# Kernel tuning notes

Measured on AMD Instinct MI355X. Metric: run time of the kernel, lower is better.

## Reference

```python
import jax, jax.numpy as jnp
import numpy as np

LAMBDA_VIOLATION = 0.5
NUM_SAMPLES = 128
EPS = 1e-09
B = 4096
K_MAX = 128
NK_MAX = 128
# unique (n, k, m) parameter combos, cycled over the batch
COMBOS = np.array([[256, 128, 3], [192, 96, 3], [224, 112, 4], [160, 80, 2]], dtype=np.int64)


def setup_inputs() -> dict:
    key = jax.random.key(0)
    k1, k2, k3 = jax.random.split(key, 3)
    y_pred = jax.random.uniform(k1, (B, 1), minval=0.5, maxval=8.0, dtype=jnp.float32)
    y_true = jax.random.uniform(k2, (B, 1), minval=0.5, maxval=8.0, dtype=jnp.float32)
    P_padded = jax.random.normal(k3, (B, K_MAX, NK_MAX), dtype=jnp.float32)
    params = jnp.asarray(COMBOS[np.arange(B) % len(COMBOS)])  # [B, 3] int64
    return {"y_pred": y_pred, "y_true": y_true, "P_padded": P_padded, "params": params}


def reference(y_pred, y_true, P_padded, params):
    # LogMSE in base 2
    log2_pred = jnp.log2(jnp.clip(y_pred, EPS))
    log2_true = jnp.log2(jnp.clip(y_true, EPS))
    loss_logmse = jnp.mean((log2_true - log2_pred) ** 2)

    batch = P_padded.shape[0]
    p_np = np.asarray(params)  # int params are concrete constants
    combos, inverse = np.unique(p_np, axis=0, return_inverse=True)

    total_penalty = jnp.asarray(0.0, dtype=y_pred.dtype)
    xkey = jax.random.key(42)
    for i in range(combos.shape[0]):
        n, k, m = int(combos[i, 0]), int(combos[i, 1]), int(combos[i, 2])
        idx = np.nonzero(inverse == i)[0]
        if m + 1 > n or k <= 0 or n - k < 0 or idx.size == 0:
            continue
        g = idx.size
        P_actual = P_padded[idx, :k, : n - k]            # [g, k, n-k]
        X = jax.random.normal(jax.random.fold_in(xkey, i), (g, NUM_SAMPLES, k), dtype=y_pred.dtype)
        # G = [I_k | P_actual]  =>  C = X @ G = [X | X @ P_actual]
        C = jnp.concatenate([X, jnp.einsum('bsk,bkp->bsp', X, P_actual)], axis=2)  # [g, S, n]
        mags = jnp.abs(C)
        top, _ = jax.lax.top_k(mags, m + 1)              # [g, S, m+1] sorted descending
        hm = top[..., 0] / (top[..., m] + EPS)           # c_max / c_m
        max_hm = jnp.max(hm, axis=1)                     # [g]
        penalty = jax.nn.relu(max_hm - y_pred[idx].squeeze(-1))
        total_penalty = total_penalty + jnp.sum(penalty)

    loss_violation = total_penalty / batch
    total_loss = loss_logmse + LAMBDA_VIOLATION * loss_violation
    return total_loss, loss_logmse, loss_violation
```

## Files before the change

kernel.cpp:

```cpp
#include <hip/hip_runtime.h>
#include <stdint.h>

typedef short bf16x8 __attribute__((ext_vector_type(8)));
typedef float f32x4 __attribute__((ext_vector_type(4)));

__host__ __device__ inline uint32_t rotl32(uint32_t v, int d) {
  return (v << d) | (v >> (32 - d));
}

__host__ __device__ inline void tf2x32(uint32_t k0, uint32_t k1,
                                       uint32_t x0, uint32_t x1,
                                       uint32_t& o0, uint32_t& o1) {
  uint32_t ks0 = k0, ks1 = k1, ks2 = k0 ^ k1 ^ 0x1BD11BDAu;
  x0 += ks0; x1 += ks1;
#define TF_R(r) { x0 += x1; x1 = rotl32(x1, (r)); x1 ^= x0; }
  TF_R(13) TF_R(15) TF_R(26) TF_R(6)
  x0 += ks1; x1 += ks2 + 1u;
  TF_R(17) TF_R(29) TF_R(16) TF_R(24)
  x0 += ks2; x1 += ks0 + 2u;
  TF_R(13) TF_R(15) TF_R(26) TF_R(6)
  x0 += ks0; x1 += ks1 + 3u;
  TF_R(17) TF_R(29) TF_R(16) TF_R(24)
  x0 += ks1; x1 += ks2 + 4u;
  TF_R(13) TF_R(15) TF_R(26) TF_R(6)
  x0 += ks2; x1 += ks0 + 5u;
#undef TF_R
  o0 = x0; o1 = x1;
}

__device__ __forceinline__ float erfinv_xla(float x) {
  float w = -__logf(fmaf(-x, x, 1.0f));
  float p;
  if (w < 5.0f) {
    w = w - 2.5f;
    p = 2.81022636e-08f;
    p = fmaf(p, w, 3.43273939e-07f);
    p = fmaf(p, w, -3.5233877e-06f);
    p = fmaf(p, w, -4.39150654e-06f);
    p = fmaf(p, w, 0.00021858087f);
    p = fmaf(p, w, -0.00125372503f);
    p = fmaf(p, w, -0.00417768164f);
    p = fmaf(p, w, 0.246640727f);
    p = fmaf(p, w, 1.50140941f);
  } else {
    w = sqrtf(w) - 3.0f;
    p = -0.000200214257f;
    p = fmaf(p, w, 0.000100950558f);
    p = fmaf(p, w, 0.00134934322f);
    p = fmaf(p, w, -0.00367342844f);
    p = fmaf(p, w, 0.00573950773f);
    p = fmaf(p, w, -0.0076224613f);
    p = fmaf(p, w, 0.00943887047f);
    p = fmaf(p, w, 1.00167406f);
    p = fmaf(p, w, 2.83297682f);
  }
  return p * x;
}

__device__ __forceinline__ float bits_to_normal(uint32_t bits) {
  uint32_t fb = (bits >> 9) | 0x3F800000u;
  float f = __uint_as_float(fb) - 1.0f;
  const float lo = -0.99999994f;
  float u = fmaf(f, 1.0f - lo, lo);
  u = fmaxf(lo, u);
  return 1.41421356f * erfinv_xla(u);
}

__device__ __forceinline__ uint32_t f2bf(float x) {
  uint32_t b = __float_as_uint(x);
  return (b + 0x7FFFu + ((b >> 16) & 1u)) >> 16;
}
__device__ __forceinline__ float bf2f_s(short h) {
  return __uint_as_float(((uint32_t)(uint16_t)h) << 16);
}

template <int T>
__device__ __forceinline__ void insT(float (&t)[T], float v) {
  float a = v;
#pragma unroll
  for (int q = 0; q < T; ++q) {
    float hi = fmaxf(t[q], a);
    a = fminf(t[q], a);
    t[q] = hi;
  }
}

template <int K, int KP, int T>
__device__ void process_combo(const float* __restrict__ Pp,
                              const float* __restrict__ yp,
                              const float* __restrict__ yt,
                              float* __restrict__ accum,
                              int ofs, uint32_t key0, uint32_t key1,
                              int rp, char* sm) {
  constexpr int KSTEPS = KP / 32;
  constexpr int NCH = (K + 31) / 32;
  constexpr int PH = K / 2;
  constexpr int ITERS = PH / 4;
  constexpr int XSTR = KP + 8;
  constexpr int XSTRU = XSTR / 2;
  constexpr int XROW_U = 64 * XSTRU;
  constexpr int BSTRU = KP / 2 + 4;
  constexpr int S_B = 32 * BSTRU * 4;
  constexpr int REGION = 2 * 64 * XSTR * 2;
  constexpr uint32_t HALF = 65536u * (uint32_t)K;

  const int tid = threadIdx.x;
  const int wave = tid >> 6;
  const int lane = tid & 63;
  const int quad = lane >> 4;
  const int l15 = lane & 15;
  const int row = wave >> 1;
  const int msub = (wave & 1) * 32;

  const int b0 = 4 * rp + ofs;
  const int b1 = 4 * (rp + 512) + ofs;

  uint32_t* Xu = (uint32_t*)sm;
  float* Xpool = (float*)(sm + REGION);
  float* wvmax = Xpool + 128 * T;
  float* maxhm = wvmax + 4;

  if (tid < 2) maxhm[tid] = 0.0f;

  for (int pass = 0; pass < 2; ++pass) {
#pragma unroll
    for (int it = 0; it < ITERS; ++it) {
      int q = it * 256 + tid;
      int s_loc = q / PH;
      int k = 2 * (q - s_loc * PH);
      uint32_t ctr = (uint32_t)((rp * 128 + pass * 64 + s_loc) * K + k);
      uint32_t o0a, o1a, o0b, o1b;
      tf2x32(key0, key1, ctr, ctr + HALF, o0a, o1a);
      tf2x32(key0, key1, ctr + 1u, ctr + 1u + HALF, o0b, o1b);
      uint32_t idx = (uint32_t)(s_loc * XSTRU + (k >> 1));
      uint32_t h0 = f2bf(bits_to_normal(o0a));
      uint32_t h1 = f2bf(bits_to_normal(o0b));
      Xu[idx] = h0 | (h1 << 16);
      h0 = f2bf(bits_to_normal(o1a));
      h1 = f2bf(bits_to_normal(o1b));
      Xu[XROW_U + idx] = h0 | (h1 << 16);
    }
    if constexpr (KP > K) {
      constexpr int PADU = (KP - K) / 2;
      for (int p = tid; p < 2 * 64 * PADU; p += 256) {
        int rs = p / PADU;
        int r = p - rs * PADU;
        Xu[rs * XSTRU + K / 2 + r] = 0;
      }
    }
    __syncthreads();

    bf16x8 ahi[2][KSTEPS];
#pragma unroll
    for (int f = 0; f < 2; ++f)
#pragma unroll
      for (int ks = 0; ks < KSTEPS; ++ks) {
        int off = ((row * 64 + msub + f * 16 + l15) * XSTR + ks * 32 + quad * 8) * 2;
        ahi[f][ks] = *(const bf16x8*)(sm + off);
      }
    {
      float t5x[2][T];
#pragma unroll
      for (int f = 0; f < 2; ++f) {
#pragma unroll
        for (int q = 0; q < T; ++q) t5x[f][q] = 0.0f;
#pragma unroll
        for (int ks = 0; ks < KSTEPS; ++ks)
#pragma unroll
          for (int j = 0; j < 8; ++j)
            insT(t5x[f], fabsf(bf2f_s(ahi[f][ks][j])));
      }
#pragma unroll
      for (int f = 0; f < 2; ++f) {
#pragma unroll
        for (int msk = 16; msk <= 32; msk <<= 1) {
          float o[T];
#pragma unroll
          for (int q = 0; q < T; ++q) o[q] = __shfl_xor(t5x[f][q], msk);
#pragma unroll
          for (int q = 0; q < T; ++q) insT(t5x[f], o[q]);
        }
      }
      if (lane < 16) {
#pragma unroll
        for (int f = 0; f < 2; ++f) {
          int slot = row * 64 + msub + f * 16 + l15;
#pragma unroll
          for (int q = 0; q < T; ++q) Xpool[slot * T + q] = t5x[f][q];
        }
      }
    }
    __syncthreads();

    float t5y[2][4][T];
#pragma unroll
    for (int f = 0; f < 2; ++f)
#pragma unroll
      for (int r = 0; r < 4; ++r)
#pragma unroll
        for (int q = 0; q < T; ++q) t5y[f][r][q] = 0.0f;

    for (int c = 0; c < NCH; ++c) {
      const int jb = c * 32;
      for (int it2 = 0; it2 < KP / 8; ++it2) {
        int q = it2 * 256 + tid;
        int j = q & 31;
        int t = q >> 5;
        int rowq = t / (KP / 2);
        int kk2 = t - rowq * (KP / 2);
        int col = jb + j;
        int kk = 2 * kk2;
        const float* Pr = Pp + (size_t)(rowq ? b1 : b0) * 16384;
        float v0 = 0.0f, v1 = 0.0f;
        if (col < K) {
          if (kk < K)     v0 = Pr[kk * 128 + col];
          if (kk + 1 < K) v1 = Pr[(kk + 1) * 128 + col];
        }
        uint32_t h0 = f2bf(v0), h1 = f2bf(v1);
        ((uint32_t*)(sm + rowq * S_B))[j * BSTRU + kk2] = h0 | (h1 << 16);
      }
      __syncthreads();

      f32x4 acc[2][2];
#pragma unroll
      for (int f = 0; f < 2; ++f)
#pragma unroll
        for (int nf = 0; nf < 2; ++nf) acc[f][nf] = (f32x4){0.f, 0.f, 0.f, 0.f};

#pragma unroll
      for (int ks = 0; ks < KSTEPS; ++ks) {
        bf16x8 bh[2];
#pragma unroll
        for (int nf = 0; nf < 2; ++nf) {
          int uidx = (nf * 16 + l15) * BSTRU + ks * 16 + quad * 4;
          bh[nf] = *(const bf16x8*)(sm + row * S_B + uidx * 4);
        }
#pragma unroll
        for (int f = 0; f < 2; ++f)
#pragma unroll
          for (int nf = 0; nf < 2; ++nf)
            acc[f][nf] = __builtin_amdgcn_mfma_f32_16x16x32_bf16(ahi[f][ks], bh[nf], acc[f][nf], 0, 0, 0);
      }
#pragma unroll
      for (int f = 0; f < 2; ++f)
#pragma unroll
        for (int nf = 0; nf < 2; ++nf)
#pragma unroll
          for (int r = 0; r < 4; ++r)
            insT(t5y[f][r], fabsf(acc[f][nf][r]));
      __syncthreads();
    }

    float wmax = 0.0f;
#pragma unroll
    for (int f = 0; f < 2; ++f)
#pragma unroll
      for (int r = 0; r < 4; ++r) {
#pragma unroll
        for (int msk = 1; msk <= 8; msk <<= 1) {
          float o[T];
#pragma unroll
          for (int q = 0; q < T; ++q) o[q] = __shfl_xor(t5y[f][r][q], msk);
#pragma unroll
          for (int q = 0; q < T; ++q) insT(t5y[f][r], o[q]);
        }
        int slot = row * 64 + msub + f * 16 + quad * 4 + r;
        const float* xp = Xpool + slot * T;
#pragma unroll
        for (int q = 0; q < T; ++q) insT(t5y[f][r], xp[q]);
        float hm = t5y[f][r][0] / (t5y[f][r][T - 1] + 1e-9f);
        wmax = fmaxf(wmax, hm);
      }
    wmax = fmaxf(wmax, __shfl_xor(wmax, 16));
    wmax = fmaxf(wmax, __shfl_xor(wmax, 32));
    if (lane == 0) wvmax[wave] = wmax;
    __syncthreads();
    if (tid < 2)
      maxhm[tid] = fmaxf(maxhm[tid], fmaxf(wvmax[2 * tid], wvmax[2 * tid + 1]));
  }

  if (tid == 0) {
    float pen = fmaxf(maxhm[0] - yp[b0], 0.0f) + fmaxf(maxhm[1] - yp[b1], 0.0f);
    atomicAdd(&accum[0], pen);
    float d0 = log2f(fmaxf(yt[b0], 1e-9f)) - log2f(fmaxf(yp[b0], 1e-9f));
    float d1 = log2f(fmaxf(yt[b1], 1e-9f)) - log2f(fmaxf(yp[b1], 1e-9f));
    atomicAdd(&accum[1], fmaf(d0, d0, d1 * d1));
  }
}

struct ComboArgs {
  int ofs[4];
  uint32_t k0[4];
  uint32_t k1[4];
};

#define SM_BYTES (34816 + 2560 + 16 + 8)

__global__ __launch_bounds__(256, 2)
void viol_kernel(const float* __restrict__ Pp, const float* __restrict__ yp,
                 const float* __restrict__ yt, float* __restrict__ accum,
                 ComboArgs ca) {
  __shared__ __align__(16) char sm[SM_BYTES];
  int i = blockIdx.x >> 9;
  int rp = blockIdx.x & 511;
  switch (i) {
    case 0: process_combo< 80,  96, 3>(Pp, yp, yt, accum, ca.ofs[0], ca.k0[0], ca.k1[0], rp, sm); break;
    case 1: process_combo< 96,  96, 4>(Pp, yp, yt, accum, ca.ofs[1], ca.k0[1], ca.k1[1], rp, sm); break;
    case 2: process_combo<112, 128, 5>(Pp, yp, yt, accum, ca.ofs[2], ca.k0[2], ca.k1[2], rp, sm); break;
    default: process_combo<128, 128, 4>(Pp, yp, yt, accum, ca.ofs[3], ca.k0[3], ca.k1[3], rp, sm); break;
  }
}

__global__ void finalize_kernel(const float* __restrict__ accum, float* __restrict__ out) {
  if (threadIdx.x == 0 && blockIdx.x == 0) {
    float viol = accum[0] / 4096.0f;
    float lm = accum[1] / 4096.0f;
    out[0] = fmaf(0.5f, viol, lm);
    out[1] = lm;
    out[2] = viol;
  }
}

extern "C" void kernel_launch(void* const* d_in, const int* in_sizes, int n_in,
                              void* d_out, int out_size, void* d_ws, size_t ws_size,
                              hipStream_t stream) {
  const float* y_pred   = (const float*)d_in[0];
  const float* y_true   = (const float*)d_in[1];
  const float* P_padded = (const float*)d_in[2];
  float* accum = (float*)d_ws;
  float* out = (float*)d_out;

  hipMemsetAsync(accum, 0, 2 * sizeof(float), stream);

  ComboArgs ca;
  const int ofs[4] = {3, 1, 2, 0};
  for (int i = 0; i < 4; ++i) {
    ca.ofs[i] = ofs[i];
    uint32_t o0, o1;
    tf2x32(0u, 42u, 0u, (uint32_t)i, o0, o1);
    ca.k0[i] = o0;
    ca.k1[i] = o1;
  }

  viol_kernel<<<2048, 256, 0, stream>>>(P_padded, y_pred, y_true, accum, ca);
  finalize_kernel<<<1, 64, 0, stream>>>(accum, out);
}
```

Baseline: 555.7 us.

## Double-buffer B tile staging, use med3 top-k insert, interleave combo blocks

The P tile loads are moved into a double-buffered LDS stage so that the next chunk's global loads and bf16 conversion are issued right after the current chunk's MFMAs. This overlaps memory latency with the top-k insertion work and drops one barrier per chunk. The top-k insert now handles its first two slots with fmed3, which shortens the dependency chain. Block indices are interleaved across the four combos so that co-resident blocks mix heavy and light template instances. In exchange, register pressure rises from the unrolled chunk loop, and the second B buffer reuses the X region of LDS.

```diff
diff --git a/kernel.cpp b/kernel.cpp
--- a/kernel.cpp
+++ b/kernel.cpp
@@ -76,12 +76,19 @@
 
 template <int T>
 __device__ __forceinline__ void insT(float (&t)[T], float v) {
-  float a = v;
-#pragma unroll
-  for (int q = 0; q < T; ++q) {
-    float hi = fmaxf(t[q], a);
-    a = fminf(t[q], a);
-    t[q] = hi;
+  if constexpr (T == 1) {
+    t[0] = fmaxf(t[0], v);
+  } else {
+    float t0o = t[0], t1o = t[1];
+    t[0] = fmaxf(t0o, v);
+    t[1] = __builtin_amdgcn_fmed3f(v, t0o, t1o);
+    float a = fminf(fminf(v, t0o), t1o);
+#pragma unroll
+    for (int q = 2; q < T; ++q) {
+      float tq = t[q];
+      t[q] = fmaxf(tq, a);
+      a = fminf(tq, a);
+    }
   }
 }
 
@@ -102,6 +109,7 @@
   constexpr int BSTRU = KP / 2 + 4;
   constexpr int S_B = 32 * BSTRU * 4;
   constexpr int REGION = 2 * 64 * XSTR * 2;
+  static_assert(4 * S_B <= REGION, "B double-buffer must fit in X region");
   constexpr uint32_t HALF = 65536u * (uint32_t)K;
 
   const int tid = threadIdx.x;
@@ -121,6 +129,28 @@
   float* maxhm = wvmax + 4;
 
   if (tid < 2) maxhm[tid] = 0.0f;
+
+  auto stageB = [&](int c, int b) {
+    const int jb = c * 32;
+#pragma unroll
+    for (int it2 = 0; it2 < KP / 8; ++it2) {
+      int q = it2 * 256 + tid;
+      int j = q & 31;
+      int t = q >> 5;
+      int rowq = t / (KP / 2);
+      int kk2 = t - rowq * (KP / 2);
+      int col = jb + j;
+      int kk = 2 * kk2;
+      const float* Pr = Pp + (size_t)(rowq ? b1 : b0) * 16384;
+      float v0 = 0.0f, v1 = 0.0f;
+      if (col < K) {
+        if (kk < K)     v0 = Pr[kk * 128 + col];
+        if (kk + 1 < K) v1 = Pr[(kk + 1) * 128 + col];
+      }
+      uint32_t h0 = f2bf(v0), h1 = f2bf(v1);
+      ((uint32_t*)(sm + (2 * b + rowq) * S_B))[j * BSTRU + kk2] = h0 | (h1 << 16);
+    }
+  };
 
   for (int pass = 0; pass < 2; ++pass) {
 #pragma unroll
@@ -192,6 +222,9 @@
     }
     __syncthreads();
 
+    stageB(0, 0);
+    __syncthreads();
+
     float t5y[2][4][T];
 #pragma unroll
     for (int f = 0; f < 2; ++f)
@@ -200,27 +233,10 @@
 #pragma unroll
         for (int q = 0; q < T; ++q) t5y[f][r][q] = 0.0f;
 
+#pragma unroll
     for (int c = 0; c < NCH; ++c) {
-      const int jb = c * 32;
-      for (int it2 = 0; it2 < KP / 8; ++it2) {
-        int q = it2 * 256 + tid;
-        int j = q & 31;
-        int t = q >> 5;
-        int rowq = t / (KP / 2);
-        int kk2 = t - rowq * (KP / 2);
-        int col = jb + j;
-        int kk = 2 * kk2;
-        const float* Pr = Pp + (size_t)(rowq ? b1 : b0) * 16384;
-        float v0 = 0.0f, v1 = 0.0f;
-        if (col < K) {
-          if (kk < K)     v0 = Pr[kk * 128 + col];
-          if (kk + 1 < K) v1 = Pr[(kk + 1) * 128 + col];
-        }
-        uint32_t h0 = f2bf(v0), h1 = f2bf(v1);
-        ((uint32_t*)(sm + rowq * S_B))[j * BSTRU + kk2] = h0 | (h1 << 16);
-      }
-      __syncthreads();
-
+      const int b = c & 1;
+      const char* bbase = sm + (2 * b + row) * S_B;
       f32x4 acc[2][2];
 #pragma unroll
       for (int f = 0; f < 2; ++f)
@@ -233,7 +249,7 @@
 #pragma unroll
         for (int nf = 0; nf < 2; ++nf) {
           int uidx = (nf * 16 + l15) * BSTRU + ks * 16 + quad * 4;
-          bh[nf] = *(const bf16x8*)(sm + row * S_B + uidx * 4);
+          bh[nf] = *(const bf16x8*)(bbase + uidx * 4);
         }
 #pragma unroll
         for (int f = 0; f < 2; ++f)
@@ -241,6 +257,8 @@
           for (int nf = 0; nf < 2; ++nf)
             acc[f][nf] = __builtin_amdgcn_mfma_f32_16x16x32_bf16(ahi[f][ks], bh[nf], acc[f][nf], 0, 0, 0);
       }
+      __builtin_amdgcn_sched_barrier(0);
+      if (c + 1 < NCH) stageB(c + 1, b ^ 1);
 #pragma unroll
       for (int f = 0; f < 2; ++f)
 #pragma unroll
@@ -248,7 +266,7 @@
 #pragma unroll
           for (int r = 0; r < 4; ++r)
             insT(t5y[f][r], fabsf(acc[f][nf][r]));
-      __syncthreads();
+      if (c + 1 < NCH) __syncthreads();
     }
 
     float wmax = 0.0f;
@@ -301,8 +319,8 @@
                  const float* __restrict__ yt, float* __restrict__ accum,
                  ComboArgs ca) {
   __shared__ __align__(16) char sm[SM_BYTES];
-  int i = blockIdx.x >> 9;
-  int rp = blockIdx.x & 511;
+  int i = blockIdx.x & 3;
+  int rp = blockIdx.x >> 2;
   switch (i) {
     case 0: process_combo< 80,  96, 3>(Pp, yp, yt, accum, ca.ofs[0], ca.k0[0], ca.k1[0], rp, sm); break;
     case 1: process_combo< 96,  96, 4>(Pp, yp, yt, accum, ca.ofs[1], ca.k0[1], ca.k1[1], rp, sm); break;
```

After: 729.2 us. 1.31x slower.
